# Optimization experiments

Hardware: AMD Instinct MI355X
Metric: run time of the kernel (lower is better)

## Reference

```python
import jax, jax.numpy as jnp
import numpy as np

N = 100_000
E = 16 * N  # avg degree 16
B = 64


def _linear_params(key, fan_in, fan_out, mode='kaiming'):
    # kaiming_uniform_ (nonlinearity='relu'): bound = sqrt(6/fan_in)
    # xavier_uniform_: bound = sqrt(6/(fan_in+fan_out))
    if mode == 'kaiming':
        bound = np.sqrt(6.0 / fan_in)
    else:
        bound = np.sqrt(6.0 / (fan_in + fan_out))
    w = jax.random.uniform(key, (fan_in, fan_out), jnp.float32, -bound, bound)
    b = jnp.zeros((fan_out,), jnp.float32)
    return w, b


def setup_inputs() -> dict:
    key = jax.random.key(0)
    ks = jax.random.split(key, 12)
    pos = jax.random.normal(ks[0], (N, 3), jnp.float32) * 10.0
    # edges: every node is a destination (deg=16 each), random sources
    src = jax.random.randint(ks[1], (E,), 0, N, jnp.int32)
    dst = jnp.repeat(jnp.arange(N, dtype=jnp.int32), E // N)
    edge_index = jnp.stack([src, dst], axis=0)  # [2, E], row0=j(src), row1=i(dst)
    batch = jnp.sort(jax.random.randint(ks[2], (N,), 0, B, jnp.int32))
    timestep = jax.random.normal(ks[3], (B,), jnp.float32)
    w1a, b1a = _linear_params(ks[4], 3 + 3, 64)
    w1b, b1b = _linear_params(ks[5], 64, 64)
    w2a, b2a = _linear_params(ks[6], 64 + 3, 64)
    w2b, b2b = _linear_params(ks[7], 64, 64)
    w3a, b3a = _linear_params(ks[8], 64 + 3, 128)
    w3b, b3b = _linear_params(ks[9], 128, 128)
    wr1, br1 = _linear_params(ks[10], 128, 64, mode='xavier')
    wr2, br2 = _linear_params(ks[11], 64, 1, mode='xavier')
    return {
        'pos': pos, 'edge_index': edge_index, 'batch': batch, 'timestep': timestep,
        'w1a': w1a, 'b1a': b1a, 'w1b': w1b, 'b1b': b1b,
        'w2a': w2a, 'b2a': b2a, 'w2b': w2b, 'b2b': b2b,
        'w3a': w3a, 'b3a': b3a, 'w3b': w3b, 'b3b': b3b,
        'wr1': wr1, 'br1': br1, 'wr2': wr2, 'br2': br2,
    }


def _pointnet_layer(h, pos, src, dst, wa, ba, wb, bb):
    # message: MLP(concat(h_j, pos_j - pos_i)); aggregate: max over incoming edges
    edge_feat = jnp.concatenate([h[src], pos[src] - pos[dst]], axis=-1)  # [E, C+3]
    msg = jnp.maximum(edge_feat @ wa + ba, 0.0) @ wb + bb               # [E, C_out]
    agg = jax.ops.segment_max(msg, dst, num_segments=N)                  # [N, C_out]
    return jnp.where(jnp.isfinite(agg), agg, 0.0)  # nodes w/o edges -> 0


def reference(pos, edge_index, batch, timestep,
              w1a, b1a, w1b, b1b, w2a, b2a, w2b, b2b,
              w3a, b3a, w3b, b3b, wr1, br1, wr2, br2):
    src, dst = edge_index[0], edge_index[1]
    h = jax.nn.relu(_pointnet_layer(pos, pos, src, dst, w1a, b1a, w1b, b1b))
    h = jax.nn.relu(_pointnet_layer(h, pos, src, dst, w2a, b2a, w2b, b2b))
    h = jax.nn.relu(_pointnet_layer(h, pos, src, dst, w3a, b3a, w3b, b3b))
    # global mean pool
    sums = jax.ops.segment_sum(h, batch, num_segments=B)          # [B, 128]
    counts = jax.ops.segment_sum(jnp.ones((h.shape[0],), h.dtype), batch, num_segments=B)
    pooled = sums / jnp.maximum(counts, 1.0)[:, None]
    out = (pooled @ wr1 + br1) @ wr2 + br2                        # [B, 1]
    return jax.nn.sigmoid(out).squeeze(-1)                        # [B]
```

## Files before the change

kernel.cpp:

```cpp
#include <hip/hip_runtime.h>
#include <math.h>

#define NNODES 100000
#define NEDGES 1600000
#define NBATCH 64
#define NTILES (NEDGES/64)

typedef __attribute__((ext_vector_type(8))) short  short8;
typedef __attribute__((ext_vector_type(4))) short  short4v;
typedef __attribute__((ext_vector_type(2))) unsigned int uint2v;
typedef __attribute__((ext_vector_type(4))) float  float4v;
typedef unsigned short ushort_t;

__device__ __forceinline__ short f2bf(float f) {
    unsigned u = __builtin_bit_cast(unsigned, f);
    u += 0x7fffu + ((u >> 16) & 1u);
    return (short)(u >> 16);
}
__device__ __forceinline__ float b2f(short s) {
    unsigned u = ((unsigned)(unsigned short)s) << 16;
    return __builtin_bit_cast(float, u);
}
__device__ __forceinline__ unsigned cvt_pk_bf16(float lo, float hi) {
    unsigned r;
    asm("v_cvt_pk_bf16_f32 %0, %1, %2" : "=v"(r) : "v"(lo), "v"(hi));
    return r;
}

__device__ __forceinline__ void barrier_lds_only() {
    asm volatile("s_waitcnt lgkmcnt(0)" ::: "memory");
    __builtin_amdgcn_sched_barrier(0);
    __builtin_amdgcn_s_barrier();
    __builtin_amdgcn_sched_barrier(0);
}

template<int CIN, int H, int O, int NWAVES, int MINW>
__global__ __launch_bounds__(NWAVES*64, MINW)
void layer_mfma(const ushort_t* __restrict__ hin, const float* __restrict__ pos,
                const int* __restrict__ srcArr,
                const float* __restrict__ wa, const float* __restrict__ ba,
                const float* __restrict__ wb, const float* __restrict__ bb,
                ushort_t* __restrict__ hout)
{
    constexpr int K1   = CIN + 3;
    constexpr int S1   = ((K1 + 31) / 32) * 32;
    constexpr int NS1  = S1 / 32;
    constexpr int NS2  = H / 32;
    constexpr int MT1  = H / 16;
    constexpr int WPM1 = NWAVES / MT1 > 0 ? NWAVES / MT1 : 1;
    constexpr int NT1  = 4 / WPM1;
    constexpr int NTIL2= O / 16;
    constexpr int WPN2 = NWAVES / NTIL2 > 0 ? NWAVES / NTIL2 : 1;
    constexpr int MT2v = 4 / WPN2;
    constexpr int RSX  = S1 + 8;
    constexpr int RSY  = H + 8;

    __shared__ short smem[64 * RSX + 64 * RSY];
    short* xs = smem;
    short* ys = smem + 64 * RSX;

    const int tid  = threadIdx.x;
    const int lane = tid & 63;
    const int w    = tid >> 6;
    const int g    = lane >> 4;
    const int c    = lane & 15;
    const int e    = tid & 63;
    const int rep  = tid >> 6;
    const int mt1  = w / WPM1;
    const int nb1  = (w % WPM1) * NT1;
    const int wnb  = w / WPN2;
    const int msub = (w % WPN2) * MT2v;
    const int STRIDE = gridDim.x;

    {
        short4v z4 = (short4v)0;
        for (int i = tid; i < (64*RSX + 64*RSY)/4; i += NWAVES*64)
            ((short4v*)smem)[i] = z4;
    }

    int srcN = srcArr[blockIdx.x * 64 + e];
    short8 pA;
    float ps0, ps1, ps2, pd0, pd1, pd2;
    auto issue = [&](int targ) {
        const int src = srcN;
        if constexpr (CIN == 3) {
            if (rep == 0) {
                ps0 = pos[src*3+0]; ps1 = pos[src*3+1]; ps2 = pos[src*3+2];
                const int node = targ*4 + (e >> 4);
                pd0 = pos[node*3+0]; pd1 = pos[node*3+1]; pd2 = pos[node*3+2];
            }
        } else {
            pA = *(const short8*)(hin + (size_t)src * CIN + rep*8);
            if (rep == 0) {
                ps0 = pos[src*3+0]; ps1 = pos[src*3+1]; ps2 = pos[src*3+2];
                const int node = targ*4 + (e >> 4);
                pd0 = pos[node*3+0]; pd1 = pos[node*3+1]; pd2 = pos[node*3+2];
            }
        }
        const int tn = min(targ + STRIDE, NTILES - 1);
        srcN = srcArr[tn*64 + e];
    };
    issue(blockIdx.x);

    short8 wah[NS1];
    float  bav[4];
    {
        const int h = mt1*16 + c;
        #pragma unroll
        for (int pk = 0; pk < NS1; ++pk) {
            short8 fh;
            #pragma unroll
            for (int j = 0; j < 8; ++j) {
                const int k = pk*32 + g*8 + j;
                fh[j] = (k < K1) ? f2bf(wa[k*H + h]) : (short)0;
            }
            wah[pk] = fh;
        }
        #pragma unroll
        for (int r = 0; r < 4; ++r) bav[r] = ba[mt1*16 + g*4 + r];
    }
    short8 wbh[NS2];
    float  bbsc;
    {
        const int o = wnb*16 + c;
        #pragma unroll
        for (int pk = 0; pk < NS2; ++pk) {
            short8 fh;
            #pragma unroll
            for (int j = 0; j < 8; ++j) {
                const int k = pk*32 + g*8 + j;
                fh[j] = f2bf(wb[k*O + o]);
            }
            wbh[pk] = fh;
        }
        bbsc = bb[o];
    }
    __syncthreads();

    for (int tile = blockIdx.x; tile < NTILES; tile += STRIDE) {
        if constexpr (CIN == 3) {
            if (rep == 0) {
                short8 hv;
                hv[0] = f2bf(ps0); hv[1] = f2bf(ps1); hv[2] = f2bf(ps2);
                hv[3] = f2bf(ps0 - pd0);
                hv[4] = f2bf(ps1 - pd1);
                hv[5] = f2bf(ps2 - pd2);
                hv[6] = 0; hv[7] = 0;
                *(short8*)(xs + e*RSX) = hv;
            }
        } else {
            *(short8*)(xs + e*RSX + rep*8) = pA;
            if (rep == 0) {
                short8 hv;
                hv[0] = f2bf(ps0 - pd0);
                hv[1] = f2bf(ps1 - pd1);
                hv[2] = f2bf(ps2 - pd2);
                hv[3]=0; hv[4]=0; hv[5]=0; hv[6]=0; hv[7]=0;
                *(short8*)(xs + e*RSX + CIN) = hv;
            }
        }
        barrier_lds_only();

        issue(min(tile + STRIDE, NTILES - 1));

        {
            float4v C1[NT1];
            #pragma unroll
            for (int ni = 0; ni < NT1; ++ni)
                #pragma unroll
                for (int r = 0; r < 4; ++r) C1[ni][r] = bav[r];
            #pragma unroll
            for (int pk = 0; pk < NS1; ++pk)
                #pragma unroll
                for (int ni = 0; ni < NT1; ++ni) {
                    short8 xh = *(const short8*)(xs + ((nb1+ni)*16 + c)*RSX + pk*32 + g*8);
                    C1[ni] = __builtin_amdgcn_mfma_f32_16x16x32_bf16(wah[pk], xh, C1[ni], 0,0,0);
                }
            #pragma unroll
            for (int ni = 0; ni < NT1; ++ni) {
                uint2v pv;
                pv[0] = cvt_pk_bf16(fmaxf(C1[ni][0], 0.f), fmaxf(C1[ni][1], 0.f));
                pv[1] = cvt_pk_bf16(fmaxf(C1[ni][2], 0.f), fmaxf(C1[ni][3], 0.f));
                *(uint2v*)(ys + ((nb1+ni)*16 + c)*RSY + mt1*16 + g*4) = pv;
            }
        }
        barrier_lds_only();

        float4v C2[MT2v];
        #pragma unroll
        for (int mi = 0; mi < MT2v; ++mi)
            #pragma unroll
            for (int r = 0; r < 4; ++r) C2[mi][r] = bbsc;
        #pragma unroll
        for (int pk = 0; pk < NS2; ++pk)
            #pragma unroll
            for (int mi = 0; mi < MT2v; ++mi) {
                short8 yh = *(const short8*)(ys + ((msub+mi)*16 + c)*RSY + pk*32 + g*8);
                C2[mi] = __builtin_amdgcn_mfma_f32_16x16x32_bf16(yh, wbh[pk], C2[mi], 0,0,0);
            }
        #pragma unroll
        for (int mi = 0; mi < MT2v; ++mi) {
            float m = fmaxf(fmaxf(C2[mi][0], C2[mi][1]),
                            fmaxf(C2[mi][2], C2[mi][3]));
            m = fmaxf(m, __shfl_xor(m, 32));
            m = fmaxf(m, __shfl_xor(m, 16));
            if (lane < 16) {
                const int node = tile*4 + msub + mi;
                hout[(size_t)node*O + wnb*16 + lane] = (ushort_t)f2bf(fmaxf(m, 0.f));
            }
        }
    }
}

__global__ void zero_k(float* __restrict__ p, int n)
{
    const int i = blockIdx.x * 256 + threadIdx.x;
    if (i < n) p[i] = 0.f;
}

__global__ void pool_k(const ushort_t* __restrict__ h3, const int* __restrict__ batch,
                       float* __restrict__ pooled, float* __restrict__ counts)
{
    const int c    = threadIdx.x & 127;
    const int half = threadIdx.x >> 7;
    const int nbeg = blockIdx.x * 128 + half * 64;
    if (nbeg >= NNODES) return;
    const int nend = min(nbeg + 64, NNODES);

    int   cur = batch[nbeg];
    float acc = 0.f;
    int   runlen = 0;
    for (int n = nbeg; n < nend; ++n) {
        const int b = batch[n];
        if (b != cur) {
            atomicAdd(pooled + cur*128 + c, acc);
            if (c == 0) atomicAdd(counts + cur, (float)runlen);
            acc = 0.f; runlen = 0; cur = b;
        }
        acc += b2f((short)h3[(size_t)n * 128 + c]);
        ++runlen;
    }
    atomicAdd(pooled + cur*128 + c, acc);
    if (c == 0) atomicAdd(counts + cur, (float)runlen);
}

__global__ void reg_k(const float* __restrict__ pooled, const float* __restrict__ counts,
                      const float* __restrict__ wr1, const float* __restrict__ br1,
                      const float* __restrict__ wr2, const float* __restrict__ br2,
                      float* __restrict__ out)
{
    const int b = blockIdx.x;
    const int h = threadIdx.x;
    const float rc = 1.f / fmaxf(counts[b], 1.f);
    float acc = br1[h];
    #pragma unroll
    for (int k = 0; k < 128; ++k)
        acc = fmaf(pooled[b*128 + k] * rc, wr1[k*64 + h], acc);
    float v = acc * wr2[h];
    #pragma unroll
    for (int s = 1; s < 64; s <<= 1)
        v += __shfl_xor(v, s);
    if (h == 0) out[b] = 1.f / (1.f + expf(-(v + br2[0])));
}

extern "C" void kernel_launch(void* const* d_in, const int* in_sizes, int n_in,
                              void* d_out, int out_size, void* d_ws, size_t ws_size,
                              hipStream_t stream)
{
    const float* pos   = (const float*)d_in[0];
    const int*   eidx  = (const int*)d_in[1];
    const int*   batch = (const int*)d_in[2];
    const float *w1a = (const float*)d_in[4],  *b1a = (const float*)d_in[5];
    const float *w1b = (const float*)d_in[6],  *b1b = (const float*)d_in[7];
    const float *w2a = (const float*)d_in[8],  *b2a = (const float*)d_in[9];
    const float *w2b = (const float*)d_in[10], *b2b = (const float*)d_in[11];
    const float *w3a = (const float*)d_in[12], *b3a = (const float*)d_in[13];
    const float *w3b = (const float*)d_in[14], *b3b = (const float*)d_in[15];
    const float *wr1 = (const float*)d_in[16], *br1 = (const float*)d_in[17];
    const float *wr2 = (const float*)d_in[18], *br2 = (const float*)d_in[19];
    const int* srcArr = eidx;

    ushort_t* h1 = (ushort_t*)d_ws;
    ushort_t* h2 = h1 + (size_t)NNODES * 64;
    ushort_t* h3 = h2 + (size_t)NNODES * 64;
    float* pooled = (float*)(h3 + (size_t)NNODES * 128);
    float* counts = pooled + NBATCH * 128;
    float* out    = (float*)d_out;

    layer_mfma<3,  64, 64, 4, 8><<<2048, dim3(256), 0, stream>>>(nullptr, pos, srcArr, w1a, b1a, w1b, b1b, h1);
    layer_mfma<64, 64, 64, 8, 6><<< 768, dim3(512), 0, stream>>>(h1,      pos, srcArr, w2a, b2a, w2b, b2b, h2);
    layer_mfma<64, 128,128,8, 6><<< 768, dim3(512), 0, stream>>>(h2,      pos, srcArr, w3a, b3a, w3b, b3b, h3);
    zero_k<<<(NBATCH*128 + NBATCH + 255)/256, dim3(256), 0, stream>>>(pooled, NBATCH*128 + NBATCH);
    pool_k<<<(NNODES + 127)/128, dim3(256), 0, stream>>>(h3, batch, pooled, counts);
    reg_k <<<NBATCH, dim3(64), 0, stream>>>(pooled, counts, wr1, br1, wr2, br2, out);
}
```

Baseline: 368.8 us.

## Give each wave 32-wide weight blocks to reuse LDS fragments across two MFMAs

```diff
diff --git a/kernel.cpp b/kernel.cpp
--- a/kernel.cpp
+++ b/kernel.cpp
@@ -25,6 +25,14 @@
     unsigned r;
     asm("v_cvt_pk_bf16_f32 %0, %1, %2" : "=v"(r) : "v"(lo), "v"(hi));
     return r;
+}
+__device__ __forceinline__ float red_groups_max(float m) {
+    unsigned a = __builtin_bit_cast(unsigned, m), b = a;
+    asm("v_permlane16_swap_b32 %0, %1" : "+v"(a), "+v"(b));
+    m = fmaxf(__builtin_bit_cast(float, a), __builtin_bit_cast(float, b));
+    a = __builtin_bit_cast(unsigned, m); b = a;
+    asm("v_permlane32_swap_b32 %0, %1" : "+v"(a), "+v"(b));
+    return fmaxf(__builtin_bit_cast(float, a), __builtin_bit_cast(float, b));
 }
 
 __device__ __forceinline__ void barrier_lds_only() {
@@ -46,12 +54,14 @@
     constexpr int S1   = ((K1 + 31) / 32) * 32;
     constexpr int NS1  = S1 / 32;
     constexpr int NS2  = H / 32;
-    constexpr int MT1  = H / 16;
-    constexpr int WPM1 = NWAVES / MT1 > 0 ? NWAVES / MT1 : 1;
-    constexpr int NT1  = 4 / WPM1;
-    constexpr int NTIL2= O / 16;
-    constexpr int WPN2 = NWAVES / NTIL2 > 0 ? NWAVES / NTIL2 : 1;
-    constexpr int MT2v = 4 / WPN2;
+    constexpr int HB1  = H / 32;
+    constexpr int EH1  = NWAVES / HB1;
+    constexpr int E1   = 64 / EH1;
+    constexpr int NT1  = E1 / 16;
+    constexpr int CB2  = O / 32;
+    constexpr int EH2  = NWAVES / CB2;
+    constexpr int E2   = 64 / EH2;
+    constexpr int MT2  = E2 / 16;
     constexpr int RSX  = S1 + 8;
     constexpr int RSY  = H + 8;
 
@@ -66,10 +76,10 @@
     const int c    = lane & 15;
     const int e    = tid & 63;
     const int rep  = tid >> 6;
-    const int mt1  = w / WPM1;
-    const int nb1  = (w % WPM1) * NT1;
-    const int wnb  = w / WPN2;
-    const int msub = (w % WPN2) * MT2v;
+    const int hb   = w / EH1;
+    const int eg1  = w % EH1;
+    const int cb2  = w / EH2;
+    const int eg2  = w % EH2;
     const int STRIDE = gridDim.x;
 
     {
@@ -102,10 +112,11 @@
     };
     issue(blockIdx.x);
 
-    short8 wah[NS1];
-    float  bav[4];
-    {
-        const int h = mt1*16 + c;
+    short8 wah[2][NS1];
+    float  bav[2][4];
+    #pragma unroll
+    for (int mt = 0; mt < 2; ++mt) {
+        const int h = hb*32 + mt*16 + c;
         #pragma unroll
         for (int pk = 0; pk < NS1; ++pk) {
             short8 fh;
@@ -114,15 +125,16 @@
                 const int k = pk*32 + g*8 + j;
                 fh[j] = (k < K1) ? f2bf(wa[k*H + h]) : (short)0;
             }
-            wah[pk] = fh;
-        }
-        #pragma unroll
-        for (int r = 0; r < 4; ++r) bav[r] = ba[mt1*16 + g*4 + r];
-    }
-    short8 wbh[NS2];
-    float  bbsc;
-    {
-        const int o = wnb*16 + c;
+            wah[mt][pk] = fh;
+        }
+        #pragma unroll
+        for (int r = 0; r < 4; ++r) bav[mt][r] = ba[hb*32 + mt*16 + g*4 + r];
+    }
+    short8 wbh[2][NS2];
+    float  bbsc[2];
+    #pragma unroll
+    for (int cb = 0; cb < 2; ++cb) {
+        const int o = cb2*32 + cb*16 + c;
         #pragma unroll
         for (int pk = 0; pk < NS2; ++pk) {
             short8 fh;
@@ -131,9 +143,9 @@
                 const int k = pk*32 + g*8 + j;
                 fh[j] = f2bf(wb[k*O + o]);
             }
-            wbh[pk] = fh;
-        }
-        bbsc = bb[o];
+            wbh[cb][pk] = fh;
+        }
+        bbsc[cb] = bb[o];
     }
     __syncthreads();
 
@@ -164,51 +176,62 @@
         issue(min(tile + STRIDE, NTILES - 1));
 
         {
-            float4v C1[NT1];
-            #pragma unroll
-            for (int ni = 0; ni < NT1; ++ni)
-                #pragma unroll
-                for (int r = 0; r < 4; ++r) C1[ni][r] = bav[r];
+            float4v C1[2][NT1];
+            #pragma unroll
+            for (int mt = 0; mt < 2; ++mt)
+                #pragma unroll
+                for (int nt = 0; nt < NT1; ++nt)
+                    #pragma unroll
+                    for (int r = 0; r < 4; ++r) C1[mt][nt][r] = bav[mt][r];
             #pragma unroll
             for (int pk = 0; pk < NS1; ++pk)
                 #pragma unroll
-                for (int ni = 0; ni < NT1; ++ni) {
-                    short8 xh = *(const short8*)(xs + ((nb1+ni)*16 + c)*RSX + pk*32 + g*8);
-                    C1[ni] = __builtin_amdgcn_mfma_f32_16x16x32_bf16(wah[pk], xh, C1[ni], 0,0,0);
+                for (int nt = 0; nt < NT1; ++nt) {
+                    short8 xh = *(const short8*)(xs + (eg1*E1 + nt*16 + c)*RSX + pk*32 + g*8);
+                    #pragma unroll
+                    for (int mt = 0; mt < 2; ++mt)
+                        C1[mt][nt] = __builtin_amdgcn_mfma_f32_16x16x32_bf16(wah[mt][pk], xh, C1[mt][nt], 0,0,0);
                 }
             #pragma unroll
-            for (int ni = 0; ni < NT1; ++ni) {
-                uint2v pv;
-                pv[0] = cvt_pk_bf16(fmaxf(C1[ni][0], 0.f), fmaxf(C1[ni][1], 0.f));
-                pv[1] = cvt_pk_bf16(fmaxf(C1[ni][2], 0.f), fmaxf(C1[ni][3], 0.f));
-                *(uint2v*)(ys + ((nb1+ni)*16 + c)*RSY + mt1*16 + g*4) = pv;
-            }
+            for (int mt = 0; mt < 2; ++mt)
+                #pragma unroll
+                for (int nt = 0; nt < NT1; ++nt) {
+                    uint2v pv;
+                    pv[0] = cvt_pk_bf16(fmaxf(C1[mt][nt][0], 0.f), fmaxf(C1[mt][nt][1], 0.f));
+                    pv[1] = cvt_pk_bf16(fmaxf(C1[mt][nt][2], 0.f), fmaxf(C1[mt][nt][3], 0.f));
+                    *(uint2v*)(ys + (eg1*E1 + nt*16 + c)*RSY + hb*32 + mt*16 + g*4) = pv;
+                }
         }
         barrier_lds_only();
 
-        float4v C2[MT2v];
-        #pragma unroll
-        for (int mi = 0; mi < MT2v; ++mi)
-            #pragma unroll
-            for (int r = 0; r < 4; ++r) C2[mi][r] = bbsc;
+        float4v C2[MT2][2];
+        #pragma unroll
+        for (int mt = 0; mt < MT2; ++mt)
+            #pragma unroll
+            for (int cb = 0; cb < 2; ++cb)
+                #pragma unroll
+                for (int r = 0; r < 4; ++r) C2[mt][cb][r] = bbsc[cb];
         #pragma unroll
         for (int pk = 0; pk < NS2; ++pk)
             #pragma unroll
-            for (int mi = 0; mi < MT2v; ++mi) {
-                short8 yh = *(const short8*)(ys + ((msub+mi)*16 + c)*RSY + pk*32 + g*8);
-                C2[mi] = __builtin_amdgcn_mfma_f32_16x16x32_bf16(yh, wbh[pk], C2[mi], 0,0,0);
-            }
-        #pragma unroll
-        for (int mi = 0; mi < MT2v; ++mi) {
-            float m = fmaxf(fmaxf(C2[mi][0], C2[mi][1]),
-                            fmaxf(C2[mi][2], C2[mi][3]));
-            m = fmaxf(m, __shfl_xor(m, 32));
-            m = fmaxf(m, __shfl_xor(m, 16));
-            if (lane < 16) {
-                const int node = tile*4 + msub + mi;
-                hout[(size_t)node*O + wnb*16 + lane] = (ushort_t)f2bf(fmaxf(m, 0.f));
-            }
-        }
+            for (int mt = 0; mt < MT2; ++mt) {
+                short8 yh = *(const short8*)(ys + (eg2*E2 + mt*16 + c)*RSY + pk*32 + g*8);
+                #pragma unroll
+                for (int cb = 0; cb < 2; ++cb)
+                    C2[mt][cb] = __builtin_amdgcn_mfma_f32_16x16x32_bf16(yh, wbh[cb][pk], C2[mt][cb], 0,0,0);
+            }
+        #pragma unroll
+        for (int mt = 0; mt < MT2; ++mt)
+            #pragma unroll
+            for (int cb = 0; cb < 2; ++cb) {
+                float m = fmaxf(fmaxf(C2[mt][cb][0], C2[mt][cb][1]),
+                                fmaxf(C2[mt][cb][2], C2[mt][cb][3]));
+                m = red_groups_max(m);
+                if (lane < 16) {
+                    const int node = tile*4 + eg2*(E2/16) + mt;
+                    hout[(size_t)node*O + cb2*32 + cb*16 + lane] = (ushort_t)f2bf(fmaxf(m, 0.f));
+                }
+            }
     }
 }
 
@@ -287,9 +310,9 @@
     float* counts = pooled + NBATCH * 128;
     float* out    = (float*)d_out;
 
-    layer_mfma<3,  64, 64, 4, 8><<<2048, dim3(256), 0, stream>>>(nullptr, pos, srcArr, w1a, b1a, w1b, b1b, h1);
-    layer_mfma<64, 64, 64, 8, 6><<< 768, dim3(512), 0, stream>>>(h1,      pos, srcArr, w2a, b2a, w2b, b2b, h2);
-    layer_mfma<64, 128,128,8, 6><<< 768, dim3(512), 0, stream>>>(h2,      pos, srcArr, w3a, b3a, w3b, b3b, h3);
+    layer_mfma<3,  64, 64, 4, 6><<<1536, dim3(256), 0, stream>>>(nullptr, pos, srcArr, w1a, b1a, w1b, b1b, h1);
+    layer_mfma<64, 64, 64, 8, 4><<< 512, dim3(512), 0, stream>>>(h1,      pos, srcArr, w2a, b2a, w2b, b2b, h2);
+    layer_mfma<64, 128,128,8, 4><<< 512, dim3(512), 0, stream>>>(h2,      pos, srcArr, w3a, b3a, w3b, b3b, h3);
     zero_k<<<(NBATCH*128 + NBATCH + 255)/256, dim3(256), 0, stream>>>(pooled, NBATCH*128 + NBATCH);
     pool_k<<<(NNODES + 127)/128, dim3(256), 0, stream>>>(h3, batch, pooled, counts);
     reg_k <<<NBATCH, dim3(64), 0, stream>>>(pooled, counts, wr1, br1, wr2, br2, out);
```

After: 357.4 us. -3.1%, faster.
